# Optimization experiments

Measured on AMD Instinct MI355X. Metric: run time of the kernel, lower is better.

## Reference

```python
import jax, jax.numpy as jnp
import numpy as np

N = 512      # n_res (act is a square pair representation [N, N, C])
C = 128      # act_dim / c_pair
I = 128      # num_intermediate_channel
EQUATION = 'ikc,jkc->ijc'  # 'outgoing' triangle multiplication
EPS = 1e-5

def _layernorm(x, g, b):
    mu = jnp.mean(x, axis=-1, keepdims=True)
    var = jnp.mean(jnp.square(x - mu), axis=-1, keepdims=True)
    return (x - mu) * jax.lax.rsqrt(var + EPS) * g + b

def setup_inputs() -> dict:
    key = jax.random.key(0)
    ks = jax.random.split(key, 12)
    s_c = 1.0 / np.sqrt(C)
    s_i = 1.0 / np.sqrt(I)
    return {
        'act': 0.1 * jax.random.normal(ks[0], (N, N, C), dtype=jnp.float32),
        'mask': (jax.random.uniform(ks[1], (N, N)) > 0.5).astype(jnp.float32),
        'ln_in_g': jnp.ones((C,), jnp.float32),
        'ln_in_b': jnp.zeros((C,), jnp.float32),
        'lp_w': s_c * jax.random.normal(ks[2], (C, I), jnp.float32),
        'lp_b': jnp.zeros((I,), jnp.float32),
        'rp_w': s_c * jax.random.normal(ks[3], (C, I), jnp.float32),
        'rp_b': jnp.zeros((I,), jnp.float32),
        'lg_w': s_c * jax.random.normal(ks[4], (C, I), jnp.float32),
        'lg_b': jnp.zeros((I,), jnp.float32),
        'rg_w': s_c * jax.random.normal(ks[5], (C, I), jnp.float32),
        'rg_b': jnp.zeros((I,), jnp.float32),
        'ln_c_g': jnp.ones((I,), jnp.float32),
        'ln_c_b': jnp.zeros((I,), jnp.float32),
        'out_w': s_i * jax.random.normal(ks[6], (I, C), jnp.float32),
        'out_b': jnp.zeros((C,), jnp.float32),
        'gate_w': s_c * jax.random.normal(ks[7], (C, C), jnp.float32),
        'gate_b': jnp.zeros((C,), jnp.float32),
    }

def reference(act, mask, ln_in_g, ln_in_b, lp_w, lp_b, rp_w, rp_b,
              lg_w, lg_b, rg_w, rg_b, ln_c_g, ln_c_b, out_w, out_b,
              gate_w, gate_b):
    m = mask[..., None]                                   # [N, N, 1]
    a = _layernorm(act, ln_in_g, ln_in_b)                 # input layernorm
    input_act = a
    # masked projections fused with sigmoid gates
    left = m * (a @ lp_w + lp_b) * jax.nn.sigmoid(a @ lg_w + lg_b)    # [N,N,I]
    right = m * (a @ rp_w + rp_b) * jax.nn.sigmoid(a @ rg_w + rg_b)   # [N,N,I]
    # triangle update: per-channel [N,N] x [N,N]^T matmul
    x = jnp.einsum(EQUATION, left, right)                 # [N,N,I]
    x = _layernorm(x, ln_c_g, ln_c_b)
    gate = jax.nn.sigmoid(input_act @ gate_w + gate_b)    # [N,N,C]
    return (x @ out_w + out_b) * gate
```

## Files before the change

kernel.cpp:

```cpp
#include <hip/hip_runtime.h>

#define NRES 512
#define N2   262144

typedef __attribute__((ext_vector_type(8))) short s16x8;
typedef __attribute__((ext_vector_type(4))) float f32x4;

__device__ __forceinline__ ushort f2bf(float x){
  union { float f; unsigned u; } v; v.f = x;
  unsigned r = (v.u + 0x7FFFu + ((v.u >> 16) & 1u)) >> 16;
  return (ushort)r;
}
__device__ __forceinline__ float bf2f(ushort h){
  union { unsigned u; float f; } v; v.u = ((unsigned)h) << 16; return v.f;
}
__device__ __forceinline__ float sigm(float x){ return 1.0f / (1.0f + __expf(-x)); }

__device__ __forceinline__ void gld_lds16(const void* g, void* lds){
  __builtin_amdgcn_global_load_lds((const __attribute__((address_space(1))) void*)g,
                                   (__attribute__((address_space(3))) void*)lds, 16, 0, 0);
}

__global__ void k0_prep(const float* __restrict__ lp, const float* __restrict__ lg,
                        const float* __restrict__ rp, const float* __restrict__ rg,
                        const float* __restrict__ gw, const float* __restrict__ ow,
                        ushort* __restrict__ Wt)
{
  const float* srcs[6] = {lp, lg, rp, rg, gw, ow};
  const float* wsrc = srcs[blockIdx.x];
  ushort* dst = Wt + blockIdx.x * 16384;
  for (int f = threadIdx.x; f < 16384; f += blockDim.x){
    int n = f >> 7, k = f & 127;
    dst[f] = f2bf(wsrc[k * 128 + n]);
  }
}

__global__ __launch_bounds__(256) void k1_proj(
    const float* __restrict__ act,  const float* __restrict__ mask,
    const float* __restrict__ ln_g, const float* __restrict__ ln_b,
    const float* __restrict__ lp_b, const float* __restrict__ lg_b,
    const float* __restrict__ rp_b, const float* __restrict__ rg_b,
    const float* __restrict__ gate_b, const ushort* __restrict__ Wt,
    ushort* __restrict__ leftg, ushort* __restrict__ rightg,
    ushort* __restrict__ gateg)
{
  __shared__ ushort Alds[128 * 136];
  __shared__ ushort Gscr[4][64 * 32];
  const int t  = threadIdx.x;
  const int p0 = blockIdx.x * 128;

  {
    const int g = t >> 5, j = t & 31;
    const float4 gv = *(const float4*)(ln_g + j * 4);
    const float4 bv = *(const float4*)(ln_b + j * 4);
    #pragma unroll
    for (int i = 0; i < 16; ++i){
      const int r = g + (i << 3);
      float4 v = *(const float4*)(act + (size_t)(p0 + r) * 128 + j * 4);
      float s = v.x + v.y + v.z + v.w;
      float q = v.x*v.x + v.y*v.y + v.z*v.z + v.w*v.w;
      #pragma unroll
      for (int m = 1; m < 32; m <<= 1){ s += __shfl_xor(s, m); q += __shfl_xor(q, m); }
      float mu = s * (1.0f / 128.0f);
      float rs = rsqrtf(q * (1.0f / 128.0f) - mu * mu + 1e-5f);
      ushort4 o;
      o.x = f2bf((v.x - mu) * rs * gv.x + bv.x);
      o.y = f2bf((v.y - mu) * rs * gv.y + bv.y);
      o.z = f2bf((v.z - mu) * rs * gv.z + bv.z);
      o.w = f2bf((v.w - mu) * rs * gv.w + bv.w);
      *(ushort4*)&Alds[r * 136 + j * 4] = o;
    }
  }
  __syncthreads();

  const int lane = t & 63, w = t >> 6;
  const int cl = lane & 15, h = lane >> 4;
  const f32x4 z = {0.f, 0.f, 0.f, 0.f};

  const float* pbias[2] = {lp_b, rp_b};
  const float* gbias[2] = {lg_b, rg_b};
  ushort* dsts[2] = {leftg, rightg};

  for (int mh = 0; mh < 2; ++mh){
    s16x8 a[4][4];
    #pragma unroll
    for (int m = 0; m < 4; ++m)
      #pragma unroll
      for (int ks = 0; ks < 4; ++ks)
        a[m][ks] = *(const s16x8*)&Alds[(mh*64 + m*16 + cl) * 136 + ks*32 + h*8];

    float mk[4][4];
    #pragma unroll
    for (int m = 0; m < 4; ++m)
      #pragma unroll
      for (int r = 0; r < 4; ++r)
        mk[m][r] = mask[p0 + mh*64 + m*16 + h*4 + r];

    #pragma unroll
    for (int grp = 0; grp < 2; ++grp){
      ushort* dst = dsts[grp];
      #pragma unroll
      for (int rep = 0; rep < 2; ++rep){
        const int c0 = (w * 2 + rep) * 16;
        const ushort* WP = Wt + (size_t)(grp * 2) * 16384 + (size_t)(c0 + cl) * 128;
        const ushort* WG = WP + 16384;
        s16x8 bP[4], bG[4];
        #pragma unroll
        for (int ks = 0; ks < 4; ++ks){
          bP[ks] = *(const s16x8*)(WP + ks*32 + h*8);
          bG[ks] = *(const s16x8*)(WG + ks*32 + h*8);
        }
        f32x4 accP[4], accG[4];
        #pragma unroll
        for (int m = 0; m < 4; ++m){ accP[m] = z; accG[m] = z; }
        #pragma unroll
        for (int ks = 0; ks < 4; ++ks)
          #pragma unroll
          for (int m = 0; m < 4; ++m){
            accP[m] = __builtin_amdgcn_mfma_f32_16x16x32_bf16(a[m][ks], bP[ks], accP[m], 0, 0, 0);
            accG[m] = __builtin_amdgcn_mfma_f32_16x16x32_bf16(a[m][ks], bG[ks], accG[m], 0, 0, 0);
          }
        const float pb = pbias[grp][c0 + cl];
        const float gb = gbias[grp][c0 + cl];
        #pragma unroll
        for (int m = 0; m < 4; ++m){
          ushort4 o;
          o.x = f2bf(mk[m][0] * (accP[m][0] + pb) * sigm(accG[m][0] + gb));
          o.y = f2bf(mk[m][1] * (accP[m][1] + pb) * sigm(accG[m][1] + gb));
          o.z = f2bf(mk[m][2] * (accP[m][2] + pb) * sigm(accG[m][2] + gb));
          o.w = f2bf(mk[m][3] * (accP[m][3] + pb) * sigm(accG[m][3] + gb));
          *(ushort4*)(dst + (size_t)(c0 + cl) * N2 + p0 + mh*64 + m*16 + h*4) = o;
        }
      }
    }

    #pragma unroll
    for (int rep = 0; rep < 2; ++rep){
      const int c0 = (w * 2 + rep) * 16;
      const ushort* W5 = Wt + (size_t)4 * 16384 + (size_t)(c0 + cl) * 128;
      s16x8 b[4];
      #pragma unroll
      for (int ks = 0; ks < 4; ++ks)
        b[ks] = *(const s16x8*)(W5 + ks*32 + h*8);
      f32x4 acc[4];
      #pragma unroll
      for (int m = 0; m < 4; ++m) acc[m] = z;
      #pragma unroll
      for (int ks = 0; ks < 4; ++ks)
        #pragma unroll
        for (int m = 0; m < 4; ++m)
          acc[m] = __builtin_amdgcn_mfma_f32_16x16x32_bf16(a[m][ks], b[ks], acc[m], 0, 0, 0);
      const float gbv = gate_b[c0 + cl];
      #pragma unroll
      for (int m = 0; m < 4; ++m)
        #pragma unroll
        for (int r = 0; r < 4; ++r)
          Gscr[w][(m*16 + h*4 + r) * 32 + rep*16 + cl] = f2bf(sigm(acc[m][r] + gbv));
    }
    #pragma unroll
    for (int u = 0; u < 4; ++u){
      const int f = u * 64 + lane;
      const int p = f >> 2, ci = f & 3;
      *(s16x8*)(gateg + (size_t)(p0 + mh*64 + p) * 128 + w*32 + ci*8) =
          *(const s16x8*)&Gscr[w][p*32 + ci*8];
    }
  }
}

__global__ __launch_bounds__(256) void k2_tri(const ushort* __restrict__ leftg,
                                              const ushort* __restrict__ rightg,
                                              float* __restrict__ X)
{
  __shared__ ushort Ab[128 * 32];
  __shared__ ushort Bb[128 * 32];
  const int t = threadIdx.x, lane = t & 63, w = t >> 6;
  const int b = blockIdx.x;
  const int c = b & 127, tile = b >> 7;
  const int tm = (tile >> 2) * 128, tn = (tile & 3) * 128;
  const ushort* Lc = leftg  + (size_t)c * N2;
  const ushort* Rc = rightg + (size_t)c * N2;
  float* Xc = X + (size_t)c * N2;
  const int wr = w >> 1, wc = w & 1, cl = lane & 15, h = lane >> 4;

  f32x4 acc[4][4];
  const f32x4 z = {0.f, 0.f, 0.f, 0.f};
  #pragma unroll
  for (int m = 0; m < 4; ++m)
    #pragma unroll
    for (int n = 0; n < 4; ++n) acc[m][n] = z;

  for (int kt = 0; kt < 16; ++kt){
    __syncthreads();
    #pragma unroll
    for (int s = 0; s < 2; ++s){
      const int q = w + 4 * s;
      const int o = q * 1024 + lane * 16;
      const int row = o >> 6, kb = o & 63;
      gld_lds16((const char*)Lc + (size_t)(tm + row) * 1024 + kt * 64 + kb,
                (char*)Ab + q * 1024);
      gld_lds16((const char*)Rc + (size_t)(tn + row) * 1024 + kt * 64 + kb,
                (char*)Bb + q * 1024);
    }
    __syncthreads();
    s16x8 a[4], bf[4];
    #pragma unroll
    for (int m = 0; m < 4; ++m)
      a[m] = *(const s16x8*)&Ab[(wr*64 + m*16 + cl) * 32 + h * 8];
    #pragma unroll
    for (int n = 0; n < 4; ++n)
      bf[n] = *(const s16x8*)&Bb[(wc*64 + n*16 + cl) * 32 + h * 8];
    #pragma unroll
    for (int m = 0; m < 4; ++m)
      #pragma unroll
      for (int n = 0; n < 4; ++n)
        acc[m][n] = __builtin_amdgcn_mfma_f32_16x16x32_bf16(a[m], bf[n], acc[m][n], 0, 0, 0);
  }

  #pragma unroll
  for (int m = 0; m < 4; ++m)
    #pragma unroll
    for (int n = 0; n < 4; ++n)
      #pragma unroll
      for (int r = 0; r < 4; ++r)
        Xc[(size_t)(tm + wr*64 + m*16 + h*4 + r) * NRES + tn + wc*64 + n*16 + cl] =
            acc[m][n][r];
}

__global__ __launch_bounds__(256) void k3_out(
    const float* __restrict__ X, const ushort* __restrict__ gateg,
    const ushort* __restrict__ Wt5,
    const float* __restrict__ ln_g, const float* __restrict__ ln_b,
    const float* __restrict__ ob, float* __restrict__ out)
{
  __shared__ ushort Alds[128 * 136];
  __shared__ ushort Wlds[128 * 136];
  __shared__ float part[8][2][128];
  __shared__ float stat[2][128];
  const int t = threadIdx.x;
  const int p0 = blockIdx.x * 128;
  const int g = t >> 5, j = t & 31;

  float4 xv[16];
  float s0 = 0, s1 = 0, s2 = 0, s3 = 0, q0 = 0, q1 = 0, q2 = 0, q3 = 0;
  #pragma unroll
  for (int i = 0; i < 16; ++i){
    const int cch = g + (i << 3);
    xv[i] = *(const float4*)(X + (size_t)cch * N2 + p0 + j * 4);
    s0 += xv[i].x; q0 += xv[i].x * xv[i].x;
    s1 += xv[i].y; q1 += xv[i].y * xv[i].y;
    s2 += xv[i].z; q2 += xv[i].z * xv[i].z;
    s3 += xv[i].w; q3 += xv[i].w * xv[i].w;
  }
  part[g][0][j*4+0] = s0; part[g][0][j*4+1] = s1;
  part[g][0][j*4+2] = s2; part[g][0][j*4+3] = s3;
  part[g][1][j*4+0] = q0; part[g][1][j*4+1] = q1;
  part[g][1][j*4+2] = q2; part[g][1][j*4+3] = q3;
  __syncthreads();
  if (t < 128){
    float s = 0, q = 0;
    #pragma unroll
    for (int gg = 0; gg < 8; ++gg){ s += part[gg][0][t]; q += part[gg][1][t]; }
    float mu = s * (1.0f / 128.0f);
    float rs = rsqrtf(q * (1.0f / 128.0f) - mu * mu + 1e-5f);
    stat[0][t] = mu; stat[1][t] = rs;
  }
  __syncthreads();
  #pragma unroll
  for (int i = 0; i < 16; ++i){
    const int cch = g + (i << 3);
    const float gc = ln_g[cch], bc = ln_b[cch];
    const int p = j * 4;
    Alds[(p+0) * 136 + cch] = f2bf((xv[i].x - stat[0][p+0]) * stat[1][p+0] * gc + bc);
    Alds[(p+1) * 136 + cch] = f2bf((xv[i].y - stat[0][p+1]) * stat[1][p+1] * gc + bc);
    Alds[(p+2) * 136 + cch] = f2bf((xv[i].z - stat[0][p+2]) * stat[1][p+2] * gc + bc);
    Alds[(p+3) * 136 + cch] = f2bf((xv[i].w - stat[0][p+3]) * stat[1][p+3] * gc + bc);
  }
  {
    #pragma unroll
    for (int u = 0; u < 8; ++u){
      int f = t + u * 256;
      int n = f >> 4, k8 = f & 15;
      *(s16x8*)&Wlds[n * 136 + k8 * 8] = *(const s16x8*)(Wt5 + f * 8);
    }
  }
  __syncthreads();

  const int lane = t & 63, w = t >> 6;
  const int wr = w >> 1, wc = w & 1, cl = lane & 15, h = lane >> 4;
  f32x4 acc[4][4];
  const f32x4 z = {0.f, 0.f, 0.f, 0.f};
  #pragma unroll
  for (int m = 0; m < 4; ++m)
    #pragma unroll
    for (int n = 0; n < 4; ++n) acc[m][n] = z;
  #pragma unroll
  for (int ks = 0; ks < 4; ++ks){
    s16x8 a[4], b[4];
    #pragma unroll
    for (int m = 0; m < 4; ++m)
      a[m] = *(const s16x8*)&Alds[(wr*64 + m*16 + cl) * 136 + ks*32 + h*8];
    #pragma unroll
    for (int n = 0; n < 4; ++n)
      b[n] = *(const s16x8*)&Wlds[(wc*64 + n*16 + cl) * 136 + ks*32 + h*8];
    #pragma unroll
    for (int m = 0; m < 4; ++m)
      #pragma unroll
      for (int n = 0; n < 4; ++n)
        acc[m][n] = __builtin_amdgcn_mfma_f32_16x16x32_bf16(a[m], b[n], acc[m][n], 0, 0, 0);
  }

  float obv[4];
  #pragma unroll
  for (int n = 0; n < 4; ++n) obv[n] = ob[wc*64 + n*16 + cl];
  #pragma unroll
  for (int m = 0; m < 4; ++m)
    #pragma unroll
    for (int n = 0; n < 4; ++n){
      const int cc = wc*64 + n*16 + cl;
      #pragma unroll
      for (int r = 0; r < 4; ++r){
        const size_t p = p0 + wr*64 + m*16 + h*4 + r;
        out[p * 128 + cc] = (acc[m][n][r] + obv[n]) * bf2f(gateg[p * 128 + cc]);
      }
    }
}

extern "C" void kernel_launch(void* const* d_in, const int* in_sizes, int n_in,
                              void* d_out, int out_size, void* d_ws, size_t ws_size,
                              hipStream_t stream)
{
  const float* act    = (const float*)d_in[0];
  const float* mask   = (const float*)d_in[1];
  const float* ln_in_g = (const float*)d_in[2];
  const float* ln_in_b = (const float*)d_in[3];
  const float* lp_w = (const float*)d_in[4];
  const float* lp_b = (const float*)d_in[5];
  const float* rp_w = (const float*)d_in[6];
  const float* rp_b = (const float*)d_in[7];
  const float* lg_w = (const float*)d_in[8];
  const float* lg_b = (const float*)d_in[9];
  const float* rg_w = (const float*)d_in[10];
  const float* rg_b = (const float*)d_in[11];
  const float* ln_c_g = (const float*)d_in[12];
  const float* ln_c_b = (const float*)d_in[13];
  const float* out_w  = (const float*)d_in[14];
  const float* out_b  = (const float*)d_in[15];
  const float* gate_w = (const float*)d_in[16];
  const float* gate_b = (const float*)d_in[17];
  float* outp = (float*)d_out;

  char* ws = (char*)d_ws;
  ushort* Wt     = (ushort*)(ws);
  ushort* leftg  = (ushort*)(ws + 196608);
  ushort* rightg = (ushort*)(ws + 196608 + 67108864ull);
  ushort* gateg  = (ushort*)(ws + 196608 + 2ull * 67108864ull);
  float*  X      = (float*) (ws + 196608 + 3ull * 67108864ull);

  k0_prep<<<dim3(6), dim3(256), 0, stream>>>(lp_w, lg_w, rp_w, rg_w, gate_w, out_w, Wt);
  k1_proj<<<dim3(2048), dim3(256), 0, stream>>>(act, mask, ln_in_g, ln_in_b,
                                                lp_b, lg_b, rp_b, rg_b, gate_b,
                                                Wt, leftg, rightg, gateg);
  k2_tri<<<dim3(2048), dim3(256), 0, stream>>>(leftg, rightg, X);
  k3_out<<<dim3(2048), dim3(256), 0, stream>>>(X, gateg, Wt + 5 * 16384,
                                               ln_c_g, ln_c_b, out_b, outp);
}
```

Measured before the change: 580.5 us.

## Double-buffer triangle matmul, store X in bf16, restructure projection kernel

New measurement: 516.5 us. -11.0%, faster.

```diff
diff --git a/kernel.cpp b/kernel.cpp
--- a/kernel.cpp
+++ b/kernel.cpp
@@ -35,7 +35,7 @@
   }
 }
 
-__global__ __launch_bounds__(256) void k1_proj(
+__global__ __launch_bounds__(512) void k1_proj(
     const float* __restrict__ act,  const float* __restrict__ mask,
     const float* __restrict__ ln_g, const float* __restrict__ ln_b,
     const float* __restrict__ lp_b, const float* __restrict__ lg_b,
@@ -45,17 +45,29 @@
     ushort* __restrict__ gateg)
 {
   __shared__ ushort Alds[128 * 136];
-  __shared__ ushort Gscr[4][64 * 32];
   const int t  = threadIdx.x;
   const int p0 = blockIdx.x * 128;
+  const int lane = t & 63, w = t >> 6;
+  const int cl = lane & 15, h = lane >> 4;
+  const int c  = w * 16 + cl;
+
+  s16x8 wf[5][4];
+  #pragma unroll
+  for (int m5 = 0; m5 < 5; ++m5)
+    #pragma unroll
+    for (int ks = 0; ks < 4; ++ks)
+      wf[m5][ks] = *(const s16x8*)(Wt + (size_t)m5 * 16384 + (size_t)c * 128 + ks * 32 + h * 8);
+  const float pb_l = lp_b[c], gb_l = lg_b[c];
+  const float pb_r = rp_b[c], gb_r = rg_b[c];
+  const float gb_g = gate_b[c];
 
   {
     const int g = t >> 5, j = t & 31;
     const float4 gv = *(const float4*)(ln_g + j * 4);
     const float4 bv = *(const float4*)(ln_b + j * 4);
     #pragma unroll
-    for (int i = 0; i < 16; ++i){
-      const int r = g + (i << 3);
+    for (int i = 0; i < 8; ++i){
+      const int r = g + (i << 4);
       float4 v = *(const float4*)(act + (size_t)(p0 + r) * 128 + j * 4);
       float s = v.x + v.y + v.z + v.w;
       float q = v.x*v.x + v.y*v.y + v.z*v.z + v.w*v.w;
@@ -73,14 +85,9 @@
   }
   __syncthreads();
 
-  const int lane = t & 63, w = t >> 6;
-  const int cl = lane & 15, h = lane >> 4;
   const f32x4 z = {0.f, 0.f, 0.f, 0.f};
 
-  const float* pbias[2] = {lp_b, rp_b};
-  const float* gbias[2] = {lg_b, rg_b};
-  ushort* dsts[2] = {leftg, rightg};
-
+  #pragma unroll
   for (int mh = 0; mh < 2; ++mh){
     s16x8 a[4][4];
     #pragma unroll
@@ -96,52 +103,49 @@
       for (int r = 0; r < 4; ++r)
         mk[m][r] = mask[p0 + mh*64 + m*16 + h*4 + r];
 
-    #pragma unroll
-    for (int grp = 0; grp < 2; ++grp){
-      ushort* dst = dsts[grp];
-      #pragma unroll
-      for (int rep = 0; rep < 2; ++rep){
-        const int c0 = (w * 2 + rep) * 16;
-        const ushort* WP = Wt + (size_t)(grp * 2) * 16384 + (size_t)(c0 + cl) * 128;
-        const ushort* WG = WP + 16384;
-        s16x8 bP[4], bG[4];
-        #pragma unroll
-        for (int ks = 0; ks < 4; ++ks){
-          bP[ks] = *(const s16x8*)(WP + ks*32 + h*8);
-          bG[ks] = *(const s16x8*)(WG + ks*32 + h*8);
-        }
-        f32x4 accP[4], accG[4];
-        #pragma unroll
-        for (int m = 0; m < 4; ++m){ accP[m] = z; accG[m] = z; }
-        #pragma unroll
-        for (int ks = 0; ks < 4; ++ks)
-          #pragma unroll
-          for (int m = 0; m < 4; ++m){
-            accP[m] = __builtin_amdgcn_mfma_f32_16x16x32_bf16(a[m][ks], bP[ks], accP[m], 0, 0, 0);
-            accG[m] = __builtin_amdgcn_mfma_f32_16x16x32_bf16(a[m][ks], bG[ks], accG[m], 0, 0, 0);
-          }
-        const float pb = pbias[grp][c0 + cl];
-        const float gb = gbias[grp][c0 + cl];
+    {
+      f32x4 accP[4], accG[4];
+      #pragma unroll
+      for (int m = 0; m < 4; ++m){ accP[m] = z; accG[m] = z; }
+      #pragma unroll
+      for (int ks = 0; ks < 4; ++ks)
         #pragma unroll
         for (int m = 0; m < 4; ++m){
-          ushort4 o;
-          o.x = f2bf(mk[m][0] * (accP[m][0] + pb) * sigm(accG[m][0] + gb));
-          o.y = f2bf(mk[m][1] * (accP[m][1] + pb) * sigm(accG[m][1] + gb));
-          o.z = f2bf(mk[m][2] * (accP[m][2] + pb) * sigm(accG[m][2] + gb));
-          o.w = f2bf(mk[m][3] * (accP[m][3] + pb) * sigm(accG[m][3] + gb));
-          *(ushort4*)(dst + (size_t)(c0 + cl) * N2 + p0 + mh*64 + m*16 + h*4) = o;
+          accP[m] = __builtin_amdgcn_mfma_f32_16x16x32_bf16(a[m][ks], wf[0][ks], accP[m], 0, 0, 0);
+          accG[m] = __builtin_amdgcn_mfma_f32_16x16x32_bf16(a[m][ks], wf[1][ks], accG[m], 0, 0, 0);
         }
+      #pragma unroll
+      for (int m = 0; m < 4; ++m){
+        ushort4 o;
+        o.x = f2bf(mk[m][0] * (accP[m][0] + pb_l) * sigm(accG[m][0] + gb_l));
+        o.y = f2bf(mk[m][1] * (accP[m][1] + pb_l) * sigm(accG[m][1] + gb_l));
+        o.z = f2bf(mk[m][2] * (accP[m][2] + pb_l) * sigm(accG[m][2] + gb_l));
+        o.w = f2bf(mk[m][3] * (accP[m][3] + pb_l) * sigm(accG[m][3] + gb_l));
+        *(ushort4*)(leftg + (size_t)c * N2 + p0 + mh*64 + m*16 + h*4) = o;
       }
     }
-
-    #pragma unroll
-    for (int rep = 0; rep < 2; ++rep){
-      const int c0 = (w * 2 + rep) * 16;
-      const ushort* W5 = Wt + (size_t)4 * 16384 + (size_t)(c0 + cl) * 128;
-      s16x8 b[4];
+    {
+      f32x4 accP[4], accG[4];
+      #pragma unroll
+      for (int m = 0; m < 4; ++m){ accP[m] = z; accG[m] = z; }
       #pragma unroll
       for (int ks = 0; ks < 4; ++ks)
-        b[ks] = *(const s16x8*)(W5 + ks*32 + h*8);
+        #pragma unroll
+        for (int m = 0; m < 4; ++m){
+          accP[m] = __builtin_amdgcn_mfma_f32_16x16x32_bf16(a[m][ks], wf[2][ks], accP[m], 0, 0, 0);
+          accG[m] = __builtin_amdgcn_mfma_f32_16x16x32_bf16(a[m][ks], wf[3][ks], accG[m], 0, 0, 0);
+        }
+      #pragma unroll
+      for (int m = 0; m < 4; ++m){
+        ushort4 o;
+        o.x = f2bf(mk[m][0] * (accP[m][0] + pb_r) * sigm(accG[m][0] + gb_r));
+        o.y = f2bf(mk[m][1] * (accP[m][1] + pb_r) * sigm(accG[m][1] + gb_r));
+        o.z = f2bf(mk[m][2] * (accP[m][2] + pb_r) * sigm(accG[m][2] + gb_r));
+        o.w = f2bf(mk[m][3] * (accP[m][3] + pb_r) * sigm(accG[m][3] + gb_r));
+        *(ushort4*)(rightg + (size_t)c * N2 + p0 + mh*64 + m*16 + h*4) = o;
+      }
+    }
+    {
       f32x4 acc[4];
       #pragma unroll
       for (int m = 0; m < 4; ++m) acc[m] = z;
@@ -149,38 +153,40 @@
       for (int ks = 0; ks < 4; ++ks)
         #pragma unroll
         for (int m = 0; m < 4; ++m)
-          acc[m] = __builtin_amdgcn_mfma_f32_16x16x32_bf16(a[m][ks], b[ks], acc[m], 0, 0, 0);
-      const float gbv = gate_b[c0 + cl];
-      #pragma unroll
-      for (int m = 0; m < 4; ++m)
-        #pragma unroll
-        for (int r = 0; r < 4; ++r)
-          Gscr[w][(m*16 + h*4 + r) * 32 + rep*16 + cl] = f2bf(sigm(acc[m][r] + gbv));
-    }
-    #pragma unroll
-    for (int u = 0; u < 4; ++u){
-      const int f = u * 64 + lane;
-      const int p = f >> 2, ci = f & 3;
-      *(s16x8*)(gateg + (size_t)(p0 + mh*64 + p) * 128 + w*32 + ci*8) =
-          *(const s16x8*)&Gscr[w][p*32 + ci*8];
+          acc[m] = __builtin_amdgcn_mfma_f32_16x16x32_bf16(a[m][ks], wf[4][ks], acc[m], 0, 0, 0);
+      #pragma unroll
+      for (int m = 0; m < 4; ++m){
+        ushort4 o;
+        o.x = f2bf(sigm(acc[m][0] + gb_g));
+        o.y = f2bf(sigm(acc[m][1] + gb_g));
+        o.z = f2bf(sigm(acc[m][2] + gb_g));
+        o.w = f2bf(sigm(acc[m][3] + gb_g));
+        *(ushort4*)(gateg + (size_t)c * N2 + p0 + mh*64 + m*16 + h*4) = o;
+      }
     }
   }
 }
 
 __global__ __launch_bounds__(256) void k2_tri(const ushort* __restrict__ leftg,
                                               const ushort* __restrict__ rightg,
-                                              float* __restrict__ X)
-{
-  __shared__ ushort Ab[128 * 32];
-  __shared__ ushort Bb[128 * 32];
+                                              ushort* __restrict__ X)
+{
+  __shared__ ushort Ab[2][128 * 32];
+  __shared__ ushort Bb[2][128 * 32];
   const int t = threadIdx.x, lane = t & 63, w = t >> 6;
   const int b = blockIdx.x;
   const int c = b & 127, tile = b >> 7;
   const int tm = (tile >> 2) * 128, tn = (tile & 3) * 128;
-  const ushort* Lc = leftg  + (size_t)c * N2;
-  const ushort* Rc = rightg + (size_t)c * N2;
-  float* Xc = X + (size_t)c * N2;
+  const char* Lc = (const char*)(leftg  + (size_t)c * N2);
+  const char* Rc = (const char*)(rightg + (size_t)c * N2);
+  ushort* Xc = X + (size_t)c * N2;
   const int wr = w >> 1, wc = w & 1, cl = lane & 15, h = lane >> 4;
+
+  const int o0 = (w    ) * 1024 + lane * 16;
+  const int o1 = (w + 4) * 1024 + lane * 16;
+  const int row0 = o0 >> 6, row1 = o1 >> 6;
+  const int sk0 = ((((o0 >> 4) & 3) ^ (row0 & 3)) << 4);
+  const int sk1 = ((((o1 >> 4) & 3) ^ (row1 & 3)) << 4);
 
   f32x4 acc[4][4];
   const f32x4 z = {0.f, 0.f, 0.f, 0.f};
@@ -189,32 +195,38 @@
     #pragma unroll
     for (int n = 0; n < 4; ++n) acc[m][n] = z;
 
-  for (int kt = 0; kt < 16; ++kt){
+  auto stage = [&](int buf, int kt){
+    gld_lds16(Lc + (size_t)(tm + row0) * 1024 + kt * 64 + sk0, (char*)&Ab[buf][0] + o0);
+    gld_lds16(Lc + (size_t)(tm + row1) * 1024 + kt * 64 + sk1, (char*)&Ab[buf][0] + o1);
+    gld_lds16(Rc + (size_t)(tn + row0) * 1024 + kt * 64 + sk0, (char*)&Bb[buf][0] + o0);
+    gld_lds16(Rc + (size_t)(tn + row1) * 1024 + kt * 64 + sk1, (char*)&Bb[buf][0] + o1);
+  };
+  const int rsw = ((h ^ (cl & 3)) << 4);
+  auto compute = [&](int buf){
+    s16x8 a2[4], b2[4];
+    #pragma unroll
+    for (int m = 0; m < 4; ++m)
+      a2[m] = *(const s16x8*)((const char*)&Ab[buf][0] + (wr*64 + m*16 + cl) * 64 + rsw);
+    #pragma unroll
+    for (int n = 0; n < 4; ++n)
+      b2[n] = *(const s16x8*)((const char*)&Bb[buf][0] + (wc*64 + n*16 + cl) * 64 + rsw);
+    #pragma unroll
+    for (int m = 0; m < 4; ++m)
+      #pragma unroll
+      for (int n = 0; n < 4; ++n)
+        acc[m][n] = __builtin_amdgcn_mfma_f32_16x16x32_bf16(a2[m], b2[n], acc[m][n], 0, 0, 0);
+  };
+
+  stage(0, 0);
+  __syncthreads();
+  int cur = 0;
+  for (int kt = 0; kt < 15; ++kt){
+    stage(cur ^ 1, kt + 1);
+    compute(cur);
     __syncthreads();
-    #pragma unroll
-    for (int s = 0; s < 2; ++s){
-      const int q = w + 4 * s;
-      const int o = q * 1024 + lane * 16;
-      const int row = o >> 6, kb = o & 63;
-      gld_lds16((const char*)Lc + (size_t)(tm + row) * 1024 + kt * 64 + kb,
-                (char*)Ab + q * 1024);
-      gld_lds16((const char*)Rc + (size_t)(tn + row) * 1024 + kt * 64 + kb,
-                (char*)Bb + q * 1024);
-    }
-    __syncthreads();
-    s16x8 a[4], bf[4];
-    #pragma unroll
-    for (int m = 0; m < 4; ++m)
-      a[m] = *(const s16x8*)&Ab[(wr*64 + m*16 + cl) * 32 + h * 8];
-    #pragma unroll
-    for (int n = 0; n < 4; ++n)
-      bf[n] = *(const s16x8*)&Bb[(wc*64 + n*16 + cl) * 32 + h * 8];
-    #pragma unroll
-    for (int m = 0; m < 4; ++m)
-      #pragma unroll
-      for (int n = 0; n < 4; ++n)
-        acc[m][n] = __builtin_amdgcn_mfma_f32_16x16x32_bf16(a[m], bf[n], acc[m][n], 0, 0, 0);
-  }
+    cur ^= 1;
+  }
+  compute(cur);
 
   #pragma unroll
   for (int m = 0; m < 4; ++m)
@@ -223,11 +235,11 @@
       #pragma unroll
       for (int r = 0; r < 4; ++r)
         Xc[(size_t)(tm + wr*64 + m*16 + h*4 + r) * NRES + tn + wc*64 + n*16 + cl] =
-            acc[m][n][r];
+            f2bf(acc[m][n][r]);
 }
 
 __global__ __launch_bounds__(256) void k3_out(
-    const float* __restrict__ X, const ushort* __restrict__ gateg,
+    const ushort* __restrict__ X, const ushort* __restrict__ gateg,
     const ushort* __restrict__ Wt5,
     const float* __restrict__ ln_g, const float* __restrict__ ln_b,
     const float* __restrict__ ob, float* __restrict__ out)
@@ -245,7 +257,9 @@
   #pragma unroll
   for (int i = 0; i < 16; ++i){
     const int cch = g + (i << 3);
-    xv[i] = *(const float4*)(X + (size_t)cch * N2 + p0 + j * 4);
+    ushort4 u4 = *(const ushort4*)(X + (size_t)cch * N2 + p0 + j * 4);
+    xv[i].x = bf2f(u4.x); xv[i].y = bf2f(u4.y);
+    xv[i].z = bf2f(u4.z); xv[i].w = bf2f(u4.w);
     s0 += xv[i].x; q0 += xv[i].x * xv[i].x;
     s1 += xv[i].y; q1 += xv[i].y * xv[i].y;
     s2 += xv[i].z; q2 += xv[i].z * xv[i].z;
@@ -275,13 +289,11 @@
     Alds[(p+2) * 136 + cch] = f2bf((xv[i].z - stat[0][p+2]) * stat[1][p+2] * gc + bc);
     Alds[(p+3) * 136 + cch] = f2bf((xv[i].w - stat[0][p+3]) * stat[1][p+3] * gc + bc);
   }
-  {
-    #pragma unroll
-    for (int u = 0; u < 8; ++u){
-      int f = t + u * 256;
-      int n = f >> 4, k8 = f & 15;
-      *(s16x8*)&Wlds[n * 136 + k8 * 8] = *(const s16x8*)(Wt5 + f * 8);
-    }
+  #pragma unroll
+  for (int u = 0; u < 8; ++u){
+    int f = t + u * 256;
+    int n = f >> 4, k8 = f & 15;
+    *(s16x8*)&Wlds[n * 136 + k8 * 8] = *(const s16x8*)(Wt5 + f * 8);
   }
   __syncthreads();
 
@@ -295,18 +307,18 @@
     for (int n = 0; n < 4; ++n) acc[m][n] = z;
   #pragma unroll
   for (int ks = 0; ks < 4; ++ks){
-    s16x8 a[4], b[4];
+    s16x8 a[4], bfr[4];
     #pragma unroll
     for (int m = 0; m < 4; ++m)
       a[m] = *(const s16x8*)&Alds[(wr*64 + m*16 + cl) * 136 + ks*32 + h*8];
     #pragma unroll
     for (int n = 0; n < 4; ++n)
-      b[n] = *(const s16x8*)&Wlds[(wc*64 + n*16 + cl) * 136 + ks*32 + h*8];
+      bfr[n] = *(const s16x8*)&Wlds[(wc*64 + n*16 + cl) * 136 + ks*32 + h*8];
     #pragma unroll
     for (int m = 0; m < 4; ++m)
       #pragma unroll
       for (int n = 0; n < 4; ++n)
-        acc[m][n] = __builtin_amdgcn_mfma_f32_16x16x32_bf16(a[m], b[n], acc[m][n], 0, 0, 0);
+        acc[m][n] = __builtin_amdgcn_mfma_f32_16x16x32_bf16(a[m], bfr[n], acc[m][n], 0, 0, 0);
   }
 
   float obv[4];
@@ -317,11 +329,12 @@
     #pragma unroll
     for (int n = 0; n < 4; ++n){
       const int cc = wc*64 + n*16 + cl;
-      #pragma unroll
-      for (int r = 0; r < 4; ++r){
-        const size_t p = p0 + wr*64 + m*16 + h*4 + r;
-        out[p * 128 + cc] = (acc[m][n][r] + obv[n]) * bf2f(gateg[p * 128 + cc]);
-      }
+      ushort4 g4 = *(const ushort4*)(gateg + (size_t)cc * N2 + p0 + wr*64 + m*16 + h*4);
+      const size_t pbase = p0 + wr*64 + m*16 + h*4;
+      out[(pbase+0) * 128 + cc] = (acc[m][n][0] + obv[n]) * bf2f(g4.x);
+      out[(pbase+1) * 128 + cc] = (acc[m][n][1] + obv[n]) * bf2f(g4.y);
+      out[(pbase+2) * 128 + cc] = (acc[m][n][2] + obv[n]) * bf2f(g4.z);
+      out[(pbase+3) * 128 + cc] = (acc[m][n][3] + obv[n]) * bf2f(g4.w);
     }
 }
 
@@ -354,10 +367,10 @@
   ushort* leftg  = (ushort*)(ws + 196608);
   ushort* rightg = (ushort*)(ws + 196608 + 67108864ull);
   ushort* gateg  = (ushort*)(ws + 196608 + 2ull * 67108864ull);
-  float*  X      = (float*) (ws + 196608 + 3ull * 67108864ull);
+  ushort* X      = (ushort*)(ws + 196608 + 3ull * 67108864ull);
 
   k0_prep<<<dim3(6), dim3(256), 0, stream>>>(lp_w, lg_w, rp_w, rg_w, gate_w, out_w, Wt);
-  k1_proj<<<dim3(2048), dim3(256), 0, stream>>>(act, mask, ln_in_g, ln_in_b,
+  k1_proj<<<dim3(2048), dim3(512), 0, stream>>>(act, mask, ln_in_g, ln_in_b,
                                                 lp_b, lg_b, rp_b, rg_b, gate_b,
                                                 Wt, leftg, rightg, gateg);
   k2_tri<<<dim3(2048), dim3(256), 0, stream>>>(leftg, rightg, X);
```
